# Performance work log

Measured on AMD Instinct MI355X. Metric: run time of the kernel, lower is better.

Reference implementation:

```python
import jax, jax.numpy as jnp
import numpy as np

D_MODEL = 1024
N_HEADS = 4  # hardcoded in the torch reshape
EPS = 1e-5


def setup_inputs() -> dict:
    key = jax.random.key(0)
    ks = jax.random.split(key, 5)
    d = D_MODEL
    x = jax.random.normal(ks[0], (4, 2048, d), dtype=jnp.float32)
    scale = 1.0 / np.sqrt(d)
    qkv_w = jax.random.normal(ks[1], (3 * d, d), dtype=jnp.float32) * scale
    qkv_b = jnp.zeros((3 * d,), dtype=jnp.float32)
    wo_w = jax.random.normal(ks[2], (d, d), dtype=jnp.float32) * scale
    wo_b = jnp.zeros((d,), dtype=jnp.float32)
    gamma = jnp.ones((d,), dtype=jnp.float32)
    beta = jnp.zeros((d,), dtype=jnp.float32)
    return {"x": x, "qkv_w": qkv_w, "qkv_b": qkv_b, "wo_w": wo_w,
            "wo_b": wo_b, "gamma": gamma, "beta": beta}


def reference(x, qkv_w, qkv_b, wo_w, wo_b, gamma, beta):
    b, s, d = x.shape
    h = N_HEADS
    hd = d // h
    # QKV projection (torch Linear: x @ W.T + b)
    qkv = x @ qkv_w.T + qkv_b                      # [b, s, 3d]
    qkv = qkv.reshape(b, s, 3, h, hd)
    qkv = jnp.transpose(qkv, (2, 0, 3, 1, 4))      # [3, b, h, s, hd]
    q, k, v = qkv[0], qkv[1], qkv[2]
    scores = jnp.einsum('bhqd,bhkd->bhqk', q, k) * (hd ** -0.5)
    attn = jax.nn.softmax(scores, axis=-1)
    out = jnp.einsum('bhqk,bhkd->bhqd', attn, v)   # [b, h, s, hd]
    out = jnp.transpose(out, (0, 2, 1, 3)).reshape(b, s, d)
    y = x + (out @ wo_w.T + wo_b)
    # LayerNorm over last dim
    mu = jnp.mean(y, axis=-1, keepdims=True)
    var = jnp.var(y, axis=-1, keepdims=True)
    return (y - mu) * jax.lax.rsqrt(var + EPS) * gamma + beta
```

## Files before the change

### kernel.cpp

```cpp
#include <hip/hip_runtime.h>
#include <hip/hip_bf16.h>

#define SEQ 2048
#define DM  1024
#define NH  4
#define HD  256

typedef __attribute__((ext_vector_type(4))) float f32x4;
typedef __attribute__((ext_vector_type(8))) short bf16x8;

__device__ __forceinline__ void gload16(const void* g, void* l) {
  __builtin_amdgcn_global_load_lds(
      (__attribute__((address_space(1))) void*)(unsigned long long)(g),
      (__attribute__((address_space(3))) void*)(l), 16, 0, 0);
}

__device__ __forceinline__ bf16x8 ldg8(const __hip_bfloat16* p) {
  return *reinterpret_cast<const bf16x8*>(p);
}

__global__ __launch_bounds__(256) void cvt_f32_bf16(const float* __restrict__ in,
                                                    __hip_bfloat16* __restrict__ out, int n4) {
  int i = blockIdx.x * 256 + threadIdx.x;
  if (i >= n4) return;
  float4 v = reinterpret_cast<const float4*>(in)[i];
  __hip_bfloat162* o2 = reinterpret_cast<__hip_bfloat162*>(out);
  o2[i * 2 + 0] = __float22bfloat162_rn(make_float2(v.x, v.y));
  o2[i * 2 + 1] = __float22bfloat162_rn(make_float2(v.z, v.w));
}

template <int EPI>
__global__ __launch_bounds__(256, 2) void gemm_bt(
    const __hip_bfloat16* __restrict__ A, const __hip_bfloat16* __restrict__ Bw,
    const float* __restrict__ bias, const float* __restrict__ resid,
    __hip_bfloat16* __restrict__ Cb, float* __restrict__ Cf, int M, int N, int K) {
  __shared__ __hip_bfloat16 ldsA[128 * 32];
  __shared__ __hip_bfloat16 ldsB[128 * 32];
  const int t = threadIdx.x;
  const int w = t >> 6, l = t & 63;
  const int lg = l >> 4, li = l & 15;
  const int m0 = blockIdx.y * 128, n0 = blockIdx.x * 128;
  const int wm = (w >> 1) * 64, wn = (w & 1) * 64;
  const int c1 = t + 256;
  const __hip_bfloat16* gA0 = A + (size_t)(m0 + (t >> 2)) * K + (t & 3) * 8;
  const __hip_bfloat16* gA1 = A + (size_t)(m0 + (c1 >> 2)) * K + (c1 & 3) * 8;
  const __hip_bfloat16* gB0 = Bw + (size_t)(n0 + (t >> 2)) * K + (t & 3) * 8;
  const __hip_bfloat16* gB1 = Bw + (size_t)(n0 + (c1 >> 2)) * K + (c1 & 3) * 8;
  __hip_bfloat16* lA0 = ldsA + t * 8;
  __hip_bfloat16* lA1 = ldsA + c1 * 8;
  __hip_bfloat16* lB0 = ldsB + t * 8;
  __hip_bfloat16* lB1 = ldsB + c1 * 8;
  f32x4 acc[4][4] = {};
  for (int k0 = 0; k0 < K; k0 += 32) {
    gload16(gA0 + k0, lA0);
    gload16(gA1 + k0, lA1);
    gload16(gB0 + k0, lB0);
    gload16(gB1 + k0, lB1);
    __syncthreads();
    bf16x8 af[4], bfr[4];
#pragma unroll
    for (int i = 0; i < 4; i++) af[i] = ldg8(&ldsA[(wm + i * 16 + li) * 32 + lg * 8]);
#pragma unroll
    for (int i = 0; i < 4; i++) bfr[i] = ldg8(&ldsB[(wn + i * 16 + li) * 32 + lg * 8]);
#pragma unroll
    for (int mi = 0; mi < 4; mi++)
#pragma unroll
      for (int ni = 0; ni < 4; ni++)
        acc[mi][ni] = __builtin_amdgcn_mfma_f32_16x16x32_bf16(af[mi], bfr[ni], acc[mi][ni], 0, 0, 0);
    __syncthreads();
  }
#pragma unroll
  for (int ni = 0; ni < 4; ni++) {
    const int col = n0 + wn + ni * 16 + li;
    const float bv = bias[col];
#pragma unroll
    for (int mi = 0; mi < 4; mi++) {
      const int rowb = m0 + wm + mi * 16 + lg * 4;
#pragma unroll
      for (int r = 0; r < 4; r++) {
        const size_t idx = (size_t)(rowb + r) * N + col;
        float v = acc[mi][ni][r] + bv;
        if (EPI) {
          Cf[idx] = v + resid[idx];
        } else {
          Cb[idx] = __float2bfloat16(v);
        }
      }
    }
  }
}

__global__ __launch_bounds__(256) void transpose_v(const short* __restrict__ qkv,
                                                   short* __restrict__ vt) {
  __shared__ short tile[32][36];
  const int t = threadIdx.x;
  const int bh = blockIdx.z, b = bh >> 2, h = bh & 3;
  const int s0 = blockIdx.x * 32, d0 = blockIdx.y * 32;
  const int sr = t >> 3, c4 = (t & 7) * 4;
  const short* src = qkv + (size_t)(b * SEQ + s0 + sr) * 3072 + 2048 + h * HD + d0 + c4;
  short4 vv = *reinterpret_cast<const short4*>(src);
  tile[sr][c4 + 0] = vv.x;
  tile[sr][c4 + 1] = vv.y;
  tile[sr][c4 + 2] = vv.z;
  tile[sr][c4 + 3] = vv.w;
  __syncthreads();
  short* dst = vt + (size_t)(bh * HD + d0 + sr) * SEQ + s0 + c4;
  short4 ov;
  ov.x = tile[c4 + 0][sr];
  ov.y = tile[c4 + 1][sr];
  ov.z = tile[c4 + 2][sr];
  ov.w = tile[c4 + 3][sr];
  *reinterpret_cast<short4*>(dst) = ov;
}

__global__ __launch_bounds__(256, 2) void flash_attn(const __hip_bfloat16* __restrict__ qkv,
                                                     const __hip_bfloat16* __restrict__ vt,
                                                     __hip_bfloat16* __restrict__ attno) {
  __shared__ __hip_bfloat16 ldsK[64 * 256];
  __shared__ __hip_bfloat16 ldsV[256 * 64];
  __shared__ __hip_bfloat16 ldsP[4][16 * 64];
  const int t = threadIdx.x, w = t >> 6, l = t & 63;
  const int lg = l >> 4, li = l & 15;
  const int qt = blockIdx.x, bh = blockIdx.y;
  const int b = bh >> 2, h = bh & 3;
  const int q0 = qt * 64 + w * 16;
  const __hip_bfloat16* Qp = qkv + (size_t)(b * SEQ + q0 + li) * 3072 + h * HD + lg * 8;
  bf16x8 aq[8];
#pragma unroll
  for (int kk = 0; kk < 8; kk++) aq[kk] = ldg8(Qp + kk * 32);
  const int krow = t >> 5;
  const int kcd = (t & 31) ^ ((t >> 5) & 7);
  const __hip_bfloat16* Kg = qkv + (size_t)(b * SEQ + krow) * 3072 + 1024 + h * HD + kcd * 8;
  const int vrow = t >> 3;
  const int vcd = (t & 7) ^ ((t >> 3) & 7);
  const __hip_bfloat16* Vg = vt + (size_t)bh * HD * SEQ + (size_t)vrow * SEQ + vcd * 8;
  __hip_bfloat16* Pw = &ldsP[w][0];
  f32x4 oacc[16] = {};
  float mst[4], lst[4];
#pragma unroll
  for (int r = 0; r < 4; r++) { mst[r] = -1e30f; lst[r] = 0.f; }
  for (int kv0 = 0; kv0 < SEQ; kv0 += 64) {
#pragma unroll
    for (int i = 0; i < 8; i++)
      gload16(Kg + (size_t)(kv0 + i * 8) * 3072, ldsK + i * 2048 + t * 8);
#pragma unroll
    for (int i = 0; i < 8; i++)
      gload16(Vg + (size_t)i * 32 * SEQ + kv0, ldsV + i * 2048 + t * 8);
    __syncthreads();
    f32x4 sacc[4] = {};
#pragma unroll
    for (int kk = 0; kk < 8; kk++) {
#pragma unroll
      for (int nf = 0; nf < 4; nf++) {
        const int r = nf * 16 + li;
        bf16x8 bk = ldg8(&ldsK[r * 256 + (((kk * 4 + lg) ^ (li & 7)) << 3)]);
        sacc[nf] = __builtin_amdgcn_mfma_f32_16x16x32_bf16(aq[kk], bk, sacc[nf], 0, 0, 0);
      }
    }
#pragma unroll
    for (int nf = 0; nf < 4; nf++)
#pragma unroll
      for (int r = 0; r < 4; r++) sacc[nf][r] *= 0.0625f;
#pragma unroll
    for (int r = 0; r < 4; r++) {
      const int q = lg * 4 + r;
      float rmax = fmaxf(fmaxf(sacc[0][r], sacc[1][r]), fmaxf(sacc[2][r], sacc[3][r]));
#pragma unroll
      for (int off = 1; off < 16; off <<= 1) rmax = fmaxf(rmax, __shfl_xor(rmax, off));
      const float mnew = fmaxf(mst[r], rmax);
      const float alpha = __expf(mst[r] - mnew);
      mst[r] = mnew;
      float p0 = __expf(sacc[0][r] - mnew);
      float p1 = __expf(sacc[1][r] - mnew);
      float p2 = __expf(sacc[2][r] - mnew);
      float p3 = __expf(sacc[3][r] - mnew);
      float ps = p0 + p1 + p2 + p3;
#pragma unroll
      for (int off = 1; off < 16; off <<= 1) ps += __shfl_xor(ps, off);
      lst[r] = lst[r] * alpha + ps;
#pragma unroll
      for (int df = 0; df < 16; df++) oacc[df][r] *= alpha;
      const int base = q * 64;
      Pw[base + (((0 + (li >> 3)) ^ (q & 7)) << 3) + (li & 7)] = __float2bfloat16(p0);
      Pw[base + (((2 + (li >> 3)) ^ (q & 7)) << 3) + (li & 7)] = __float2bfloat16(p1);
      Pw[base + (((4 + (li >> 3)) ^ (q & 7)) << 3) + (li & 7)] = __float2bfloat16(p2);
      Pw[base + (((6 + (li >> 3)) ^ (q & 7)) << 3) + (li & 7)] = __float2bfloat16(p3);
    }
    asm volatile("" ::: "memory");
#pragma unroll
    for (int ks = 0; ks < 2; ks++) {
      bf16x8 pa = ldg8(&Pw[li * 64 + (((ks * 4 + lg) ^ (li & 7)) << 3)]);
#pragma unroll
      for (int df = 0; df < 16; df++) {
        const int d = df * 16 + li;
        bf16x8 bv = ldg8(&ldsV[d * 64 + (((ks * 4 + lg) ^ (li & 7)) << 3)]);
        oacc[df] = __builtin_amdgcn_mfma_f32_16x16x32_bf16(pa, bv, oacc[df], 0, 0, 0);
      }
    }
    __syncthreads();
  }
  const size_t orow = (size_t)(b * SEQ + qt * 64 + w * 16 + lg * 4);
#pragma unroll
  for (int df = 0; df < 16; df++)
#pragma unroll
    for (int r = 0; r < 4; r++) {
      float v = oacc[df][r] / lst[r];
      attno[(orow + r) * DM + h * HD + df * 16 + li] = __float2bfloat16(v);
    }
}

__global__ __launch_bounds__(256) void layernorm_k(const float* __restrict__ y,
                                                   const float* __restrict__ gamma,
                                                   const float* __restrict__ beta,
                                                   float* __restrict__ out) {
  const int w = threadIdx.x >> 6, l = threadIdx.x & 63;
  const size_t row = (size_t)blockIdx.x * 4 + w;
  const float4* yp = reinterpret_cast<const float4*>(y + row * DM);
  float4 v[4];
  float s = 0.f, s2 = 0.f;
#pragma unroll
  for (int i = 0; i < 4; i++) {
    v[i] = yp[i * 64 + l];
    s += v[i].x + v[i].y + v[i].z + v[i].w;
    s2 += v[i].x * v[i].x + v[i].y * v[i].y + v[i].z * v[i].z + v[i].w * v[i].w;
  }
#pragma unroll
  for (int off = 1; off < 64; off <<= 1) {
    s += __shfl_xor(s, off);
    s2 += __shfl_xor(s2, off);
  }
  const float mu = s * (1.f / 1024.f);
  const float rs = rsqrtf(s2 * (1.f / 1024.f) - mu * mu + 1e-5f);
  const float4* gp = reinterpret_cast<const float4*>(gamma);
  const float4* bp = reinterpret_cast<const float4*>(beta);
  float4* op = reinterpret_cast<float4*>(out + row * DM);
#pragma unroll
  for (int i = 0; i < 4; i++) {
    float4 g = gp[i * 64 + l], bb = bp[i * 64 + l];
    float4 o;
    o.x = (v[i].x - mu) * rs * g.x + bb.x;
    o.y = (v[i].y - mu) * rs * g.y + bb.y;
    o.z = (v[i].z - mu) * rs * g.z + bb.z;
    o.w = (v[i].w - mu) * rs * g.w + bb.w;
    op[i * 64 + l] = o;
  }
}

extern "C" void kernel_launch(void* const* d_in, const int* in_sizes, int n_in,
                              void* d_out, int out_size, void* d_ws, size_t ws_size,
                              hipStream_t stream) {
  const float* x     = (const float*)d_in[0];
  const float* qkv_w = (const float*)d_in[1];
  const float* qkv_b = (const float*)d_in[2];
  const float* wo_w  = (const float*)d_in[3];
  const float* wo_b  = (const float*)d_in[4];
  const float* gamma = (const float*)d_in[5];
  const float* beta  = (const float*)d_in[6];
  float* out = (float*)d_out;
  char* ws = (char*)d_ws;
  __hip_bfloat16* xbf   = (__hip_bfloat16*)(ws);
  __hip_bfloat16* qkvwb = (__hip_bfloat16*)(ws + 16777216);
  __hip_bfloat16* wowb  = (__hip_bfloat16*)(ws + 23068672);
  __hip_bfloat16* qkv   = (__hip_bfloat16*)(ws + 25165824);
  float*          yb    = (float*)(ws + 25165824);
  __hip_bfloat16* vt    = (__hip_bfloat16*)(ws + 75497472);
  __hip_bfloat16* attno = xbf;

  cvt_f32_bf16<<<8192, 256, 0, stream>>>(x, xbf, 2097152);
  cvt_f32_bf16<<<3072, 256, 0, stream>>>(qkv_w, qkvwb, 786432);
  cvt_f32_bf16<<<1024, 256, 0, stream>>>(wo_w, wowb, 262144);
  gemm_bt<0><<<dim3(24, 64), 256, 0, stream>>>(xbf, qkvwb, qkv_b, nullptr, qkv, nullptr,
                                               8192, 3072, 1024);
  transpose_v<<<dim3(64, 8, 16), 256, 0, stream>>>((const short*)qkv, (short*)vt);
  flash_attn<<<dim3(32, 16), 256, 0, stream>>>(qkv, vt, attno);
  gemm_bt<1><<<dim3(8, 64), 256, 0, stream>>>(attno, wowb, wo_b, x, nullptr, yb,
                                              8192, 1024, 1024);
  layernorm_k<<<2048, 256, 0, stream>>>(yb, gamma, beta, out);
}
```

Measured before the change: 264.1 us.

## Double-buffer K/V tiles in flash attention with lazy softmax rescaling

Restructures the flash attention loop to use 32-key tiles held in two LDS buffers, so global-to-LDS loads for the next tile are issued while the current tile is computed. It also skips the output rescale unless the running max grows by more than a threshold, remaps block indices to spread batch/head work across the grid, and replaces the per-element division with a reciprocal multiply. LDS use per block stays roughly the same, but tiles are smaller, so there are more loop iterations and barriers. The lazy max update lets exponent arguments reach up to 8 above the stored max, which could lose precision or overflow for unusual score ranges.

```diff
diff --git a/kernel.cpp b/kernel.cpp
--- a/kernel.cpp
+++ b/kernel.cpp
@@ -116,95 +116,102 @@
 __global__ __launch_bounds__(256, 2) void flash_attn(const __hip_bfloat16* __restrict__ qkv,
                                                      const __hip_bfloat16* __restrict__ vt,
                                                      __hip_bfloat16* __restrict__ attno) {
-  __shared__ __hip_bfloat16 ldsK[64 * 256];
-  __shared__ __hip_bfloat16 ldsV[256 * 64];
-  __shared__ __hip_bfloat16 ldsP[4][16 * 64];
-  const int t = threadIdx.x, w = t >> 6, l = t & 63;
+  __shared__ __hip_bfloat16 ldsK[2][32 * 256];
+  __shared__ __hip_bfloat16 ldsV[2][256 * 32];
+  __shared__ __hip_bfloat16 ldsP[4][16 * 32];
+  const int tid = threadIdx.x, w = tid >> 6, l = tid & 63;
   const int lg = l >> 4, li = l & 15;
-  const int qt = blockIdx.x, bh = blockIdx.y;
+  const int bid = blockIdx.x;
+  const int qt = bid >> 4;
+  const int bh = (bid & 7) * 2 + ((bid >> 3) & 1);
   const int b = bh >> 2, h = bh & 3;
   const int q0 = qt * 64 + w * 16;
   const __hip_bfloat16* Qp = qkv + (size_t)(b * SEQ + q0 + li) * 3072 + h * HD + lg * 8;
   bf16x8 aq[8];
 #pragma unroll
   for (int kk = 0; kk < 8; kk++) aq[kk] = ldg8(Qp + kk * 32);
-  const int krow = t >> 5;
-  const int kcd = (t & 31) ^ ((t >> 5) & 7);
-  const __hip_bfloat16* Kg = qkv + (size_t)(b * SEQ + krow) * 3072 + 1024 + h * HD + kcd * 8;
-  const int vrow = t >> 3;
-  const int vcd = (t & 7) ^ ((t >> 3) & 7);
-  const __hip_bfloat16* Vg = vt + (size_t)bh * HD * SEQ + (size_t)vrow * SEQ + vcd * 8;
+  const int kcd = (tid & 31) ^ ((tid >> 5) & 7);
+  const __hip_bfloat16* Kg = qkv + (size_t)(b * SEQ + (tid >> 5)) * 3072 + 1024 + h * HD + kcd * 8;
+  const int vcd = (tid & 3) ^ ((tid >> 4) & 3);
+  const __hip_bfloat16* Vg = vt + (size_t)bh * HD * SEQ + (size_t)(tid >> 2) * SEQ + vcd * 8;
   __hip_bfloat16* Pw = &ldsP[w][0];
   f32x4 oacc[16] = {};
   float mst[4], lst[4];
 #pragma unroll
   for (int r = 0; r < 4; r++) { mst[r] = -1e30f; lst[r] = 0.f; }
-  for (int kv0 = 0; kv0 < SEQ; kv0 += 64) {
-#pragma unroll
-    for (int i = 0; i < 8; i++)
-      gload16(Kg + (size_t)(kv0 + i * 8) * 3072, ldsK + i * 2048 + t * 8);
-#pragma unroll
-    for (int i = 0; i < 8; i++)
-      gload16(Vg + (size_t)i * 32 * SEQ + kv0, ldsV + i * 2048 + t * 8);
-    __syncthreads();
-    f32x4 sacc[4] = {};
+#pragma unroll
+  for (int i = 0; i < 4; i++) gload16(Kg + (size_t)(i * 8) * 3072, &ldsK[0][i * 2048 + tid * 8]);
+#pragma unroll
+  for (int i = 0; i < 4; i++) gload16(Vg + (size_t)(i * 64) * SEQ, &ldsV[0][i * 2048 + tid * 8]);
+  __syncthreads();
+#pragma unroll 2
+  for (int t = 0; t < SEQ / 32; ++t) {
+    const int cur = t & 1;
+    if (t + 1 < SEQ / 32) {
+      const int nk = (t + 1) * 32;
+#pragma unroll
+      for (int i = 0; i < 4; i++)
+        gload16(Kg + (size_t)(nk + i * 8) * 3072, &ldsK[cur ^ 1][i * 2048 + tid * 8]);
+#pragma unroll
+      for (int i = 0; i < 4; i++)
+        gload16(Vg + (size_t)(i * 64) * SEQ + nk, &ldsV[cur ^ 1][i * 2048 + tid * 8]);
+    }
+    const __hip_bfloat16* Kb = &ldsK[cur][0];
+    const __hip_bfloat16* Vb = &ldsV[cur][0];
+    f32x4 sacc[2] = {};
 #pragma unroll
     for (int kk = 0; kk < 8; kk++) {
 #pragma unroll
-      for (int nf = 0; nf < 4; nf++) {
+      for (int nf = 0; nf < 2; nf++) {
         const int r = nf * 16 + li;
-        bf16x8 bk = ldg8(&ldsK[r * 256 + (((kk * 4 + lg) ^ (li & 7)) << 3)]);
+        bf16x8 bk = ldg8(&Kb[r * 256 + (((kk * 4 + lg) ^ (li & 7)) << 3)]);
         sacc[nf] = __builtin_amdgcn_mfma_f32_16x16x32_bf16(aq[kk], bk, sacc[nf], 0, 0, 0);
       }
     }
 #pragma unroll
-    for (int nf = 0; nf < 4; nf++)
-#pragma unroll
-      for (int r = 0; r < 4; r++) sacc[nf][r] *= 0.0625f;
-#pragma unroll
     for (int r = 0; r < 4; r++) {
+      const float s0 = sacc[0][r] * 0.0625f;
+      const float s1 = sacc[1][r] * 0.0625f;
+      float rmax = fmaxf(s0, s1);
+#pragma unroll
+      for (int off = 1; off < 16; off <<= 1) rmax = fmaxf(rmax, __shfl_xor(rmax, off));
+      if (rmax > mst[r] + 8.f) {
+        const float alpha = __expf(mst[r] - rmax);
+        mst[r] = rmax;
+        lst[r] *= alpha;
+#pragma unroll
+        for (int df = 0; df < 16; df++) oacc[df][r] *= alpha;
+      }
+      const float p0 = __expf(s0 - mst[r]);
+      const float p1 = __expf(s1 - mst[r]);
+      float ps = p0 + p1;
+#pragma unroll
+      for (int off = 1; off < 16; off <<= 1) ps += __shfl_xor(ps, off);
+      lst[r] += ps;
       const int q = lg * 4 + r;
-      float rmax = fmaxf(fmaxf(sacc[0][r], sacc[1][r]), fmaxf(sacc[2][r], sacc[3][r]));
-#pragma unroll
-      for (int off = 1; off < 16; off <<= 1) rmax = fmaxf(rmax, __shfl_xor(rmax, off));
-      const float mnew = fmaxf(mst[r], rmax);
-      const float alpha = __expf(mst[r] - mnew);
-      mst[r] = mnew;
-      float p0 = __expf(sacc[0][r] - mnew);
-      float p1 = __expf(sacc[1][r] - mnew);
-      float p2 = __expf(sacc[2][r] - mnew);
-      float p3 = __expf(sacc[3][r] - mnew);
-      float ps = p0 + p1 + p2 + p3;
-#pragma unroll
-      for (int off = 1; off < 16; off <<= 1) ps += __shfl_xor(ps, off);
-      lst[r] = lst[r] * alpha + ps;
-#pragma unroll
-      for (int df = 0; df < 16; df++) oacc[df][r] *= alpha;
-      const int base = q * 64;
-      Pw[base + (((0 + (li >> 3)) ^ (q & 7)) << 3) + (li & 7)] = __float2bfloat16(p0);
-      Pw[base + (((2 + (li >> 3)) ^ (q & 7)) << 3) + (li & 7)] = __float2bfloat16(p1);
-      Pw[base + (((4 + (li >> 3)) ^ (q & 7)) << 3) + (li & 7)] = __float2bfloat16(p2);
-      Pw[base + (((6 + (li >> 3)) ^ (q & 7)) << 3) + (li & 7)] = __float2bfloat16(p3);
+      const int swzp = (q >> 1) & 3;
+      Pw[q * 32 + (((0 + (li >> 3)) ^ swzp) << 3) + (li & 7)] = __float2bfloat16(p0);
+      Pw[q * 32 + (((2 + (li >> 3)) ^ swzp) << 3) + (li & 7)] = __float2bfloat16(p1);
     }
     asm volatile("" ::: "memory");
-#pragma unroll
-    for (int ks = 0; ks < 2; ks++) {
-      bf16x8 pa = ldg8(&Pw[li * 64 + (((ks * 4 + lg) ^ (li & 7)) << 3)]);
-#pragma unroll
-      for (int df = 0; df < 16; df++) {
-        const int d = df * 16 + li;
-        bf16x8 bv = ldg8(&ldsV[d * 64 + (((ks * 4 + lg) ^ (li & 7)) << 3)]);
-        oacc[df] = __builtin_amdgcn_mfma_f32_16x16x32_bf16(pa, bv, oacc[df], 0, 0, 0);
-      }
+    bf16x8 pa = ldg8(&Pw[li * 32 + ((lg ^ ((li >> 1) & 3)) << 3)]);
+#pragma unroll
+    for (int df = 0; df < 16; df++) {
+      const int d = df * 16 + li;
+      bf16x8 bv = ldg8(&Vb[d * 32 + ((lg ^ (li >> 2)) << 3)]);
+      oacc[df] = __builtin_amdgcn_mfma_f32_16x16x32_bf16(pa, bv, oacc[df], 0, 0, 0);
     }
     __syncthreads();
   }
+  const float inv0 = 1.f / lst[0], inv1 = 1.f / lst[1];
+  const float inv2 = 1.f / lst[2], inv3 = 1.f / lst[3];
+  const float inv[4] = {inv0, inv1, inv2, inv3};
   const size_t orow = (size_t)(b * SEQ + qt * 64 + w * 16 + lg * 4);
 #pragma unroll
   for (int df = 0; df < 16; df++)
 #pragma unroll
     for (int r = 0; r < 4; r++) {
-      float v = oacc[df][r] / lst[r];
+      float v = oacc[df][r] * inv[r];
       attno[(orow + r) * DM + h * HD + df * 16 + li] = __float2bfloat16(v);
     }
 }
@@ -272,7 +279,7 @@
   gemm_bt<0><<<dim3(24, 64), 256, 0, stream>>>(xbf, qkvwb, qkv_b, nullptr, qkv, nullptr,
                                                8192, 3072, 1024);
   transpose_v<<<dim3(64, 8, 16), 256, 0, stream>>>((const short*)qkv, (short*)vt);
-  flash_attn<<<dim3(32, 16), 256, 0, stream>>>(qkv, vt, attno);
+  flash_attn<<<512, 256, 0, stream>>>(qkv, vt, attno);
   gemm_bt<1><<<dim3(8, 64), 256, 0, stream>>>(attno, wowb, wo_b, x, nullptr, yb,
                                               8192, 1024, 1024);
   layernorm_k<<<2048, 256, 0, stream>>>(yb, gamma, beta, out);
```

New measurement: 291.7 us. 1.1x slower.

## Double-buffer K/V tiles, double per-wave query rows, and defer softmax rescaling

Applied to the files above, without the earlier changes.

Flash attention now processes 32 query rows per wave (128 per block), so each K/V tile loaded into LDS is reused by twice as many query rows. K/V tiles are double-buffered, with the next tile's global-to-LDS loads issued before computing on the current one. Rescaling of the running max is skipped unless the new max exceeds the old by more than 8, and row sums are accumulated with an MFMA against a ones vector instead of shuffle reductions. The grid becomes 256 blocks with a remapped block-to-head order, occupancy drops to one block per CU, and register pressure rises with the doubled accumulators.

```diff
diff --git a/kernel.cpp b/kernel.cpp
--- a/kernel.cpp
+++ b/kernel.cpp
@@ -113,100 +113,131 @@
   *reinterpret_cast<short4*>(dst) = ov;
 }
 
-__global__ __launch_bounds__(256, 2) void flash_attn(const __hip_bfloat16* __restrict__ qkv,
+__global__ __launch_bounds__(256, 1) void flash_attn(const __hip_bfloat16* __restrict__ qkv,
                                                      const __hip_bfloat16* __restrict__ vt,
                                                      __hip_bfloat16* __restrict__ attno) {
-  __shared__ __hip_bfloat16 ldsK[64 * 256];
-  __shared__ __hip_bfloat16 ldsV[256 * 64];
-  __shared__ __hip_bfloat16 ldsP[4][16 * 64];
-  const int t = threadIdx.x, w = t >> 6, l = t & 63;
+  __shared__ __hip_bfloat16 ldsK[2][64 * 256];
+  __shared__ __hip_bfloat16 ldsV[2][256 * 64];
+  __shared__ __hip_bfloat16 ldsP[4][32 * 64];
+  const int tid = threadIdx.x, w = tid >> 6, l = tid & 63;
   const int lg = l >> 4, li = l & 15;
-  const int qt = blockIdx.x, bh = blockIdx.y;
+  const int bid = blockIdx.x;
+  const int qt = bid >> 4;
+  const int bh = (bid & 7) * 2 + ((bid >> 3) & 1);
   const int b = bh >> 2, h = bh & 3;
-  const int q0 = qt * 64 + w * 16;
-  const __hip_bfloat16* Qp = qkv + (size_t)(b * SEQ + q0 + li) * 3072 + h * HD + lg * 8;
-  bf16x8 aq[8];
-#pragma unroll
-  for (int kk = 0; kk < 8; kk++) aq[kk] = ldg8(Qp + kk * 32);
-  const int krow = t >> 5;
-  const int kcd = (t & 31) ^ ((t >> 5) & 7);
-  const __hip_bfloat16* Kg = qkv + (size_t)(b * SEQ + krow) * 3072 + 1024 + h * HD + kcd * 8;
-  const int vrow = t >> 3;
-  const int vcd = (t & 7) ^ ((t >> 3) & 7);
-  const __hip_bfloat16* Vg = vt + (size_t)bh * HD * SEQ + (size_t)vrow * SEQ + vcd * 8;
+  const int q0 = qt * 128 + w * 32;
+  bf16x8 aq[2][8];
+#pragma unroll
+  for (int a = 0; a < 2; a++) {
+    const __hip_bfloat16* Qp =
+        qkv + (size_t)(b * SEQ + q0 + a * 16 + li) * 3072 + h * HD + lg * 8;
+#pragma unroll
+    for (int kk = 0; kk < 8; kk++) aq[a][kk] = ldg8(Qp + kk * 32);
+  }
+  const int kcd = (tid & 31) ^ ((tid >> 5) & 7);
+  const __hip_bfloat16* Kg = qkv + (size_t)(b * SEQ + (tid >> 5)) * 3072 + 1024 + h * HD + kcd * 8;
+  const int vcd = (tid & 7) ^ ((tid >> 3) & 7);
+  const __hip_bfloat16* Vg = vt + (size_t)bh * HD * SEQ + (size_t)(tid >> 3) * SEQ + vcd * 8;
   __hip_bfloat16* Pw = &ldsP[w][0];
-  f32x4 oacc[16] = {};
-  float mst[4], lst[4];
-#pragma unroll
-  for (int r = 0; r < 4; r++) { mst[r] = -1e30f; lst[r] = 0.f; }
-  for (int kv0 = 0; kv0 < SEQ; kv0 += 64) {
-#pragma unroll
-    for (int i = 0; i < 8; i++)
-      gload16(Kg + (size_t)(kv0 + i * 8) * 3072, ldsK + i * 2048 + t * 8);
-#pragma unroll
-    for (int i = 0; i < 8; i++)
-      gload16(Vg + (size_t)i * 32 * SEQ + kv0, ldsV + i * 2048 + t * 8);
+  f32x4 oacc[2][16] = {};
+  f32x4 lacc[2] = {};
+  float mst[2][4];
+#pragma unroll
+  for (int a = 0; a < 2; a++)
+#pragma unroll
+    for (int r = 0; r < 4; r++) mst[a][r] = -1e30f;
+#pragma unroll
+  for (int i = 0; i < 8; i++) gload16(Kg + (size_t)(i * 8) * 3072, &ldsK[0][i * 2048 + tid * 8]);
+#pragma unroll
+  for (int i = 0; i < 8; i++) gload16(Vg + (size_t)(i * 32) * SEQ, &ldsV[0][i * 2048 + tid * 8]);
+  __syncthreads();
+#pragma unroll 2
+  for (int t = 0; t < SEQ / 64; ++t) {
+    const int cur = t & 1;
+    if (t + 1 < SEQ / 64) {
+      const int nk = (t + 1) * 64;
+#pragma unroll
+      for (int i = 0; i < 8; i++)
+        gload16(Kg + (size_t)(nk + i * 8) * 3072, &ldsK[cur ^ 1][i * 2048 + tid * 8]);
+#pragma unroll
+      for (int i = 0; i < 8; i++)
+        gload16(Vg + (size_t)(i * 32) * SEQ + nk, &ldsV[cur ^ 1][i * 2048 + tid * 8]);
+    }
+    const __hip_bfloat16* Kb = &ldsK[cur][0];
+    const __hip_bfloat16* Vb = &ldsV[cur][0];
+    f32x4 sacc[2][4] = {};
+#pragma unroll
+    for (int kk = 0; kk < 8; kk++) {
+#pragma unroll
+      for (int nf = 0; nf < 4; nf++) {
+        bf16x8 bk = ldg8(&Kb[(nf * 16 + li) * 256 + (((kk * 4 + lg) ^ (li & 7)) << 3)]);
+        sacc[0][nf] = __builtin_amdgcn_mfma_f32_16x16x32_bf16(aq[0][kk], bk, sacc[0][nf], 0, 0, 0);
+        sacc[1][nf] = __builtin_amdgcn_mfma_f32_16x16x32_bf16(aq[1][kk], bk, sacc[1][nf], 0, 0, 0);
+      }
+    }
+#pragma unroll
+    for (int a = 0; a < 2; a++) {
+#pragma unroll
+      for (int r = 0; r < 4; r++) {
+        const float s0 = sacc[a][0][r] * 0.0625f;
+        const float s1 = sacc[a][1][r] * 0.0625f;
+        const float s2 = sacc[a][2][r] * 0.0625f;
+        const float s3 = sacc[a][3][r] * 0.0625f;
+        float rmax = fmaxf(fmaxf(s0, s1), fmaxf(s2, s3));
+#pragma unroll
+        for (int off = 1; off < 16; off <<= 1) rmax = fmaxf(rmax, __shfl_xor(rmax, off));
+        if (rmax > mst[a][r] + 8.f) {
+          const float alpha = __expf(mst[a][r] - rmax);
+          mst[a][r] = rmax;
+          lacc[a][r] *= alpha;
+#pragma unroll
+          for (int df = 0; df < 16; df++) oacc[a][df][r] *= alpha;
+        }
+        const float p0 = __expf(s0 - mst[a][r]);
+        const float p1 = __expf(s1 - mst[a][r]);
+        const float p2 = __expf(s2 - mst[a][r]);
+        const float p3 = __expf(s3 - mst[a][r]);
+        const int q = a * 16 + lg * 4 + r;
+        const int base = q * 64;
+        Pw[base + (((0 + (li >> 3)) ^ (q & 7)) << 3) + (li & 7)] = __float2bfloat16(p0);
+        Pw[base + (((2 + (li >> 3)) ^ (q & 7)) << 3) + (li & 7)] = __float2bfloat16(p1);
+        Pw[base + (((4 + (li >> 3)) ^ (q & 7)) << 3) + (li & 7)] = __float2bfloat16(p2);
+        Pw[base + (((6 + (li >> 3)) ^ (q & 7)) << 3) + (li & 7)] = __float2bfloat16(p3);
+      }
+    }
+    asm volatile("" ::: "memory");
+    bf16x8 ones;
+#pragma unroll
+    for (int j = 0; j < 8; j++) ones[j] = (short)0x3F80;
+#pragma unroll
+    for (int ks = 0; ks < 2; ks++) {
+      bf16x8 pa0 = ldg8(&Pw[li * 64 + (((ks * 4 + lg) ^ (li & 7)) << 3)]);
+      bf16x8 pa1 = ldg8(&Pw[(16 + li) * 64 + (((ks * 4 + lg) ^ (li & 7)) << 3)]);
+      lacc[0] = __builtin_amdgcn_mfma_f32_16x16x32_bf16(pa0, ones, lacc[0], 0, 0, 0);
+      lacc[1] = __builtin_amdgcn_mfma_f32_16x16x32_bf16(pa1, ones, lacc[1], 0, 0, 0);
+#pragma unroll
+      for (int df = 0; df < 16; df++) {
+        bf16x8 bv = ldg8(&Vb[(df * 16 + li) * 64 + (((ks * 4 + lg) ^ (li & 7)) << 3)]);
+        oacc[0][df] = __builtin_amdgcn_mfma_f32_16x16x32_bf16(pa0, bv, oacc[0][df], 0, 0, 0);
+        oacc[1][df] = __builtin_amdgcn_mfma_f32_16x16x32_bf16(pa1, bv, oacc[1][df], 0, 0, 0);
+      }
+    }
     __syncthreads();
-    f32x4 sacc[4] = {};
-#pragma unroll
-    for (int kk = 0; kk < 8; kk++) {
-#pragma unroll
-      for (int nf = 0; nf < 4; nf++) {
-        const int r = nf * 16 + li;
-        bf16x8 bk = ldg8(&ldsK[r * 256 + (((kk * 4 + lg) ^ (li & 7)) << 3)]);
-        sacc[nf] = __builtin_amdgcn_mfma_f32_16x16x32_bf16(aq[kk], bk, sacc[nf], 0, 0, 0);
-      }
-    }
-#pragma unroll
-    for (int nf = 0; nf < 4; nf++)
-#pragma unroll
-      for (int r = 0; r < 4; r++) sacc[nf][r] *= 0.0625f;
-#pragma unroll
-    for (int r = 0; r < 4; r++) {
-      const int q = lg * 4 + r;
-      float rmax = fmaxf(fmaxf(sacc[0][r], sacc[1][r]), fmaxf(sacc[2][r], sacc[3][r]));
-#pragma unroll
-      for (int off = 1; off < 16; off <<= 1) rmax = fmaxf(rmax, __shfl_xor(rmax, off));
-      const float mnew = fmaxf(mst[r], rmax);
-      const float alpha = __expf(mst[r] - mnew);
-      mst[r] = mnew;
-      float p0 = __expf(sacc[0][r] - mnew);
-      float p1 = __expf(sacc[1][r] - mnew);
-      float p2 = __expf(sacc[2][r] - mnew);
-      float p3 = __expf(sacc[3][r] - mnew);
-      float ps = p0 + p1 + p2 + p3;
-#pragma unroll
-      for (int off = 1; off < 16; off <<= 1) ps += __shfl_xor(ps, off);
-      lst[r] = lst[r] * alpha + ps;
-#pragma unroll
-      for (int df = 0; df < 16; df++) oacc[df][r] *= alpha;
-      const int base = q * 64;
-      Pw[base + (((0 + (li >> 3)) ^ (q & 7)) << 3) + (li & 7)] = __float2bfloat16(p0);
-      Pw[base + (((2 + (li >> 3)) ^ (q & 7)) << 3) + (li & 7)] = __float2bfloat16(p1);
-      Pw[base + (((4 + (li >> 3)) ^ (q & 7)) << 3) + (li & 7)] = __float2bfloat16(p2);
-      Pw[base + (((6 + (li >> 3)) ^ (q & 7)) << 3) + (li & 7)] = __float2bfloat16(p3);
-    }
-    asm volatile("" ::: "memory");
-#pragma unroll
-    for (int ks = 0; ks < 2; ks++) {
-      bf16x8 pa = ldg8(&Pw[li * 64 + (((ks * 4 + lg) ^ (li & 7)) << 3)]);
-#pragma unroll
-      for (int df = 0; df < 16; df++) {
-        const int d = df * 16 + li;
-        bf16x8 bv = ldg8(&ldsV[d * 64 + (((ks * 4 + lg) ^ (li & 7)) << 3)]);
-        oacc[df] = __builtin_amdgcn_mfma_f32_16x16x32_bf16(pa, bv, oacc[df], 0, 0, 0);
-      }
-    }
-    __syncthreads();
-  }
-  const size_t orow = (size_t)(b * SEQ + qt * 64 + w * 16 + lg * 4);
-#pragma unroll
-  for (int df = 0; df < 16; df++)
-#pragma unroll
-    for (int r = 0; r < 4; r++) {
-      float v = oacc[df][r] / lst[r];
-      attno[(orow + r) * DM + h * HD + df * 16 + li] = __float2bfloat16(v);
-    }
+  }
+  const size_t orow = (size_t)(b * SEQ + q0);
+#pragma unroll
+  for (int a = 0; a < 2; a++) {
+    float inv[4];
+#pragma unroll
+    for (int r = 0; r < 4; r++) inv[r] = 1.f / lacc[a][r];
+#pragma unroll
+    for (int df = 0; df < 16; df++)
+#pragma unroll
+      for (int r = 0; r < 4; r++) {
+        float v = oacc[a][df][r] * inv[r];
+        attno[(orow + a * 16 + lg * 4 + r) * DM + h * HD + df * 16 + li] = __float2bfloat16(v);
+      }
+  }
 }
 
 __global__ __launch_bounds__(256) void layernorm_k(const float* __restrict__ y,
@@ -272,7 +303,7 @@
   gemm_bt<0><<<dim3(24, 64), 256, 0, stream>>>(xbf, qkvwb, qkv_b, nullptr, qkv, nullptr,
                                                8192, 3072, 1024);
   transpose_v<<<dim3(64, 8, 16), 256, 0, stream>>>((const short*)qkv, (short*)vt);
-  flash_attn<<<dim3(32, 16), 256, 0, stream>>>(qkv, vt, attno);
+  flash_attn<<<256, 256, 0, stream>>>(qkv, vt, attno);
   gemm_bt<1><<<dim3(8, 64), 256, 0, stream>>>(attno, wowb, wo_b, x, nullptr, yb,
                                               8192, 1024, 1024);
   layernorm_k<<<2048, 256, 0, stream>>>(yb, gamma, beta, out);
```

New measurement: 303.9 us. +15.1%, slower.

## Rewrite flash attention with 32x32 MFMA, split-KV wave groups, and register-held P

Applied to the files above, without the earlier changes.

The flash attention kernel now launches 512 threads per block covering 128 queries. Two wave groups each take half of the KV sequence and merge their partial outputs through LDS at the end. The QK^T and PV products use 32x32x16 MFMAs with K and V as the A operand, so the probabilities stay in registers and are exchanged through lane shuffles instead of an LDS round trip. Rescaling is lazy, applied only when the row max grows by more than 8. This also adds an XCD-aware block-to-head mapping. The costs are higher register pressure from 8 f32x16 accumulators, more LDS from the double KV buffers, and an extra cross-group reduction step.

```diff
diff --git a/kernel.cpp b/kernel.cpp
--- a/kernel.cpp
+++ b/kernel.cpp
@@ -7,6 +7,7 @@
 #define HD  256
 
 typedef __attribute__((ext_vector_type(4))) float f32x4;
+typedef __attribute__((ext_vector_type(16))) float f32x16;
 typedef __attribute__((ext_vector_type(8))) short bf16x8;
 
 __device__ __forceinline__ void gload16(const void* g, void* l) {
@@ -17,6 +18,16 @@
 
 __device__ __forceinline__ bf16x8 ldg8(const __hip_bfloat16* p) {
   return *reinterpret_cast<const bf16x8*>(p);
+}
+
+__device__ __forceinline__ unsigned pack2(float a, float b) {
+  __hip_bfloat162 t = __float22bfloat162_rn(make_float2(a, b));
+  return *reinterpret_cast<unsigned*>(&t);
+}
+
+__device__ __forceinline__ short bfbits(float x) {
+  __hip_bfloat16 h = __float2bfloat16(x);
+  return *reinterpret_cast<short*>(&h);
 }
 
 __global__ __launch_bounds__(256) void cvt_f32_bf16(const float* __restrict__ in,
@@ -113,100 +124,155 @@
   *reinterpret_cast<short4*>(dst) = ov;
 }
 
-__global__ __launch_bounds__(256, 2) void flash_attn(const __hip_bfloat16* __restrict__ qkv,
+__global__ __launch_bounds__(512, 2) void flash_attn(const __hip_bfloat16* __restrict__ qkv,
                                                      const __hip_bfloat16* __restrict__ vt,
                                                      __hip_bfloat16* __restrict__ attno) {
-  __shared__ __hip_bfloat16 ldsK[64 * 256];
-  __shared__ __hip_bfloat16 ldsV[256 * 64];
-  __shared__ __hip_bfloat16 ldsP[4][16 * 64];
-  const int t = threadIdx.x, w = t >> 6, l = t & 63;
-  const int lg = l >> 4, li = l & 15;
-  const int qt = blockIdx.x, bh = blockIdx.y;
+  __shared__ __hip_bfloat16 ldsK[2][64 * 256];
+  __shared__ __hip_bfloat16 ldsV[2][256 * 64];
+  __shared__ float mlx[8][2][32];
+  const int tid = threadIdx.x, w = tid >> 6, l = tid & 63;
+  const int l31 = l & 31, hi = l >> 5;
+  const int g = w >> 2, gt = tid & 255;
+  const int bid = blockIdx.x;
+  const int bh = (bid & 7) * 2 + ((bid >> 3) & 1);
+  const int qt = bid >> 4;
   const int b = bh >> 2, h = bh & 3;
-  const int q0 = qt * 64 + w * 16;
-  const __hip_bfloat16* Qp = qkv + (size_t)(b * SEQ + q0 + li) * 3072 + h * HD + lg * 8;
-  bf16x8 aq[8];
-#pragma unroll
-  for (int kk = 0; kk < 8; kk++) aq[kk] = ldg8(Qp + kk * 32);
-  const int krow = t >> 5;
-  const int kcd = (t & 31) ^ ((t >> 5) & 7);
-  const __hip_bfloat16* Kg = qkv + (size_t)(b * SEQ + krow) * 3072 + 1024 + h * HD + kcd * 8;
-  const int vrow = t >> 3;
-  const int vcd = (t & 7) ^ ((t >> 3) & 7);
-  const __hip_bfloat16* Vg = vt + (size_t)bh * HD * SEQ + (size_t)vrow * SEQ + vcd * 8;
-  __hip_bfloat16* Pw = &ldsP[w][0];
-  f32x4 oacc[16] = {};
-  float mst[4], lst[4];
-#pragma unroll
-  for (int r = 0; r < 4; r++) { mst[r] = -1e30f; lst[r] = 0.f; }
-  for (int kv0 = 0; kv0 < SEQ; kv0 += 64) {
+  const int qsub = qt * 128 + (w & 3) * 32;
+  const int kvbase = g * 1024;
+  bf16x8 bq[16];
+  {
+    const __hip_bfloat16* Qp = qkv + (size_t)(b * SEQ + qsub + l31) * 3072 + h * HD + hi * 8;
+#pragma unroll
+    for (int kst = 0; kst < 16; kst++) bq[kst] = ldg8(Qp + kst * 16);
+  }
+  const int kcd = (gt & 31) ^ ((gt >> 5) & 7);
+  const __hip_bfloat16* Kg =
+      qkv + (size_t)(b * SEQ + kvbase + (gt >> 5)) * 3072 + 1024 + h * HD + kcd * 8;
+  const int vcd = (gt & 7) ^ ((gt >> 3) & 7);
+  const __hip_bfloat16* Vg =
+      vt + (size_t)bh * HD * SEQ + (size_t)(gt >> 3) * SEQ + kvbase + vcd * 8;
+  __hip_bfloat16* lK = &ldsK[g][0];
+  __hip_bfloat16* lV = &ldsV[g][0];
+
+  f32x16 oacc[8] = {};
+  float m_run = -1e30f, lsum = 0.f;
+
+  for (int t = 0; t < 16; ++t) {
 #pragma unroll
     for (int i = 0; i < 8; i++)
-      gload16(Kg + (size_t)(kv0 + i * 8) * 3072, ldsK + i * 2048 + t * 8);
+      gload16(Kg + (size_t)(t * 64 + i * 8) * 3072, lK + i * 2048 + gt * 8);
 #pragma unroll
     for (int i = 0; i < 8; i++)
-      gload16(Vg + (size_t)i * 32 * SEQ + kv0, ldsV + i * 2048 + t * 8);
+      gload16(Vg + (size_t)(i * 32) * SEQ + t * 64, lV + i * 2048 + gt * 8);
     __syncthreads();
-    f32x4 sacc[4] = {};
-#pragma unroll
-    for (int kk = 0; kk < 8; kk++) {
-#pragma unroll
-      for (int nf = 0; nf < 4; nf++) {
-        const int r = nf * 16 + li;
-        bf16x8 bk = ldg8(&ldsK[r * 256 + (((kk * 4 + lg) ^ (li & 7)) << 3)]);
-        sacc[nf] = __builtin_amdgcn_mfma_f32_16x16x32_bf16(aq[kk], bk, sacc[nf], 0, 0, 0);
-      }
-    }
-#pragma unroll
-    for (int nf = 0; nf < 4; nf++)
-#pragma unroll
-      for (int r = 0; r < 4; r++) sacc[nf][r] *= 0.0625f;
-#pragma unroll
-    for (int r = 0; r < 4; r++) {
-      const int q = lg * 4 + r;
-      float rmax = fmaxf(fmaxf(sacc[0][r], sacc[1][r]), fmaxf(sacc[2][r], sacc[3][r]));
-#pragma unroll
-      for (int off = 1; off < 16; off <<= 1) rmax = fmaxf(rmax, __shfl_xor(rmax, off));
-      const float mnew = fmaxf(mst[r], rmax);
-      const float alpha = __expf(mst[r] - mnew);
-      mst[r] = mnew;
-      float p0 = __expf(sacc[0][r] - mnew);
-      float p1 = __expf(sacc[1][r] - mnew);
-      float p2 = __expf(sacc[2][r] - mnew);
-      float p3 = __expf(sacc[3][r] - mnew);
-      float ps = p0 + p1 + p2 + p3;
-#pragma unroll
-      for (int off = 1; off < 16; off <<= 1) ps += __shfl_xor(ps, off);
-      lst[r] = lst[r] * alpha + ps;
-#pragma unroll
-      for (int df = 0; df < 16; df++) oacc[df][r] *= alpha;
-      const int base = q * 64;
-      Pw[base + (((0 + (li >> 3)) ^ (q & 7)) << 3) + (li & 7)] = __float2bfloat16(p0);
-      Pw[base + (((2 + (li >> 3)) ^ (q & 7)) << 3) + (li & 7)] = __float2bfloat16(p1);
-      Pw[base + (((4 + (li >> 3)) ^ (q & 7)) << 3) + (li & 7)] = __float2bfloat16(p2);
-      Pw[base + (((6 + (li >> 3)) ^ (q & 7)) << 3) + (li & 7)] = __float2bfloat16(p3);
-    }
-    asm volatile("" ::: "memory");
-#pragma unroll
-    for (int ks = 0; ks < 2; ks++) {
-      bf16x8 pa = ldg8(&Pw[li * 64 + (((ks * 4 + lg) ^ (li & 7)) << 3)]);
-#pragma unroll
-      for (int df = 0; df < 16; df++) {
-        const int d = df * 16 + li;
-        bf16x8 bv = ldg8(&ldsV[d * 64 + (((ks * 4 + lg) ^ (li & 7)) << 3)]);
-        oacc[df] = __builtin_amdgcn_mfma_f32_16x16x32_bf16(pa, bv, oacc[df], 0, 0, 0);
+#pragma unroll
+    for (int t32 = 0; t32 < 2; t32++) {
+      f32x16 sa = {}, sb = {};
+      const int krow = t32 * 32 + l31;
+      const int ksw = krow & 7;
+#pragma unroll
+      for (int kst = 0; kst < 8; kst++) {
+        bf16x8 aka = ldg8(&lK[krow * 256 + (((4 * kst + hi) ^ ksw) << 3)]);
+        bf16x8 akb = ldg8(&lK[krow * 256 + (((4 * kst + 2 + hi) ^ ksw) << 3)]);
+        sa = __builtin_amdgcn_mfma_f32_32x32x16_bf16(aka, bq[2 * kst], sa, 0, 0, 0);
+        sb = __builtin_amdgcn_mfma_f32_32x32x16_bf16(akb, bq[2 * kst + 1], sb, 0, 0, 0);
+      }
+#pragma unroll
+      for (int r = 0; r < 16; r++) sa[r] = (sa[r] + sb[r]) * 0.0625f;
+      float rmax = sa[0];
+#pragma unroll
+      for (int r = 1; r < 16; r++) rmax = fmaxf(rmax, sa[r]);
+      rmax = fmaxf(rmax, __shfl_xor(rmax, 32));
+      if (rmax > m_run + 8.f) {
+        const float alpha = __expf(m_run - rmax);
+        m_run = rmax;
+        lsum *= alpha;
+#pragma unroll
+        for (int dt = 0; dt < 8; dt++)
+#pragma unroll
+          for (int r = 0; r < 16; r++) oacc[dt][r] *= alpha;
+      }
+      float psum = 0.f;
+#pragma unroll
+      for (int r = 0; r < 16; r++) {
+        sa[r] = __expf(sa[r] - m_run);
+        psum += sa[r];
+      }
+      lsum += psum + __shfl_xor(psum, 32);
+#pragma unroll
+      for (int s16 = 0; s16 < 2; s16++) {
+        const int rb = s16 * 8;
+        unsigned a0 = pack2(sa[rb + 0], sa[rb + 1]);
+        unsigned a1 = pack2(sa[rb + 2], sa[rb + 3]);
+        unsigned b0 = pack2(sa[rb + 4], sa[rb + 5]);
+        unsigned b1 = pack2(sa[rb + 6], sa[rb + 7]);
+        unsigned s0 = (unsigned)__shfl_xor((int)(hi ? a0 : b0), 32);
+        unsigned s1 = (unsigned)__shfl_xor((int)(hi ? a1 : b1), 32);
+        union { unsigned u[4]; bf16x8 v; } pw;
+        pw.u[0] = hi ? s0 : a0;
+        pw.u[1] = hi ? s1 : a1;
+        pw.u[2] = hi ? b0 : s0;
+        pw.u[3] = hi ? b1 : s1;
+        const int vch = t32 * 4 + s16 * 2 + hi;
+#pragma unroll
+        for (int dt = 0; dt < 8; dt++) {
+          const int drow = dt * 32 + l31;
+          bf16x8 av = ldg8(&lV[drow * 64 + ((vch ^ (drow & 7)) << 3)]);
+          oacc[dt] = __builtin_amdgcn_mfma_f32_32x32x16_bf16(av, pw.v, oacc[dt], 0, 0, 0);
+        }
       }
     }
     __syncthreads();
   }
-  const size_t orow = (size_t)(b * SEQ + qt * 64 + w * 16 + lg * 4);
-#pragma unroll
-  for (int df = 0; df < 16; df++)
-#pragma unroll
-    for (int r = 0; r < 4; r++) {
-      float v = oacc[df][r] / lst[r];
-      attno[(orow + r) * DM + h * HD + df * 16 + li] = __float2bfloat16(v);
-    }
+  if (l < 32) {
+    mlx[w][0][l] = m_run;
+    mlx[w][1][l] = lsum;
+  }
+  __syncthreads();
+  {
+    const float m_o = mlx[w ^ 4][0][l31];
+    const float l_o = mlx[w ^ 4][1][l31];
+    const float mm = fmaxf(m_run, m_o);
+    const float e_s = __expf(m_run - mm), e_o = __expf(m_o - mm);
+    const float wgt = e_s / (e_s * lsum + e_o * l_o);
+#pragma unroll
+    for (int dt = 0; dt < 8; dt++)
+#pragma unroll
+      for (int r = 0; r < 16; r++) oacc[dt][r] *= wgt;
+  }
+  const int pair = w & 3;
+  float* xch = pair < 2 ? reinterpret_cast<float*>(&ldsK[0][0]) + pair * 8192
+                        : reinterpret_cast<float*>(&ldsV[0][0]) + (pair - 2) * 8192;
+  if (g == 0) {
+#pragma unroll
+    for (int dt = 0; dt < 8; dt++)
+#pragma unroll
+      for (int rq = 0; rq < 4; rq++) {
+        const int dch = dt * 8 + 2 * rq + hi;
+        f32x4 v;
+#pragma unroll
+        for (int i = 0; i < 4; i++) v[i] = oacc[dt][4 * rq + i];
+        *reinterpret_cast<f32x4*>(&xch[l31 * 256 + ((dch ^ (l31 & 7)) << 2)]) = v;
+      }
+  }
+  __syncthreads();
+  if (g == 1) {
+    const size_t rowb = (size_t)(b * SEQ + qsub + l31) * DM + h * HD;
+#pragma unroll
+    for (int dt = 0; dt < 8; dt++)
+#pragma unroll
+      for (int rq = 0; rq < 4; rq++) {
+        const int dch = dt * 8 + 2 * rq + hi;
+        f32x4 p = *reinterpret_cast<const f32x4*>(&xch[l31 * 256 + ((dch ^ (l31 & 7)) << 2)]);
+        short4 sv;
+        sv.x = bfbits(p[0] + oacc[dt][4 * rq + 0]);
+        sv.y = bfbits(p[1] + oacc[dt][4 * rq + 1]);
+        sv.z = bfbits(p[2] + oacc[dt][4 * rq + 2]);
+        sv.w = bfbits(p[3] + oacc[dt][4 * rq + 3]);
+        *reinterpret_cast<short4*>(
+            reinterpret_cast<short*>(attno + rowb + dt * 32 + 8 * rq + 4 * hi)) = sv;
+      }
+  }
 }
 
 __global__ __launch_bounds__(256) void layernorm_k(const float* __restrict__ y,
@@ -272,7 +338,7 @@
   gemm_bt<0><<<dim3(24, 64), 256, 0, stream>>>(xbf, qkvwb, qkv_b, nullptr, qkv, nullptr,
                                                8192, 3072, 1024);
   transpose_v<<<dim3(64, 8, 16), 256, 0, stream>>>((const short*)qkv, (short*)vt);
-  flash_attn<<<dim3(32, 16), 256, 0, stream>>>(qkv, vt, attno);
+  flash_attn<<<256, 512, 0, stream>>>(qkv, vt, attno);
   gemm_bt<1><<<dim3(8, 64), 256, 0, stream>>>(attno, wowb, wo_b, x, nullptr, yb,
                                               8192, 1024, 1024);
   layernorm_k<<<2048, 256, 0, stream>>>(yb, gamma, beta, out);
```

After: 255.3 us. 3.3% less time.
